# Kernel tuning notes

Hardware: AMD Instinct MI355X
Metric: run time of the kernel (lower is better)

Reference implementation:

```python
import jax, jax.numpy as jnp
import numpy as np

LN2 = 0.693147
TARGET_MEAN = 200.0
TARGET_STD = 40.0
BUFFER_SIZE = 1000
TARGET_LOG_MEAN = float(np.log2(TARGET_MEAN))
TARGET_LOG_STD = TARGET_STD / (TARGET_MEAN * LN2)
BLOCK = 33_554_432  # 2**25 pitch frames


def setup_inputs() -> dict:
    key = jax.random.key(0)
    k1, k2 = jax.random.split(key)
    u = jax.random.uniform(k1, (BLOCK,), dtype=jnp.float32)
    unvoiced = jax.random.uniform(k2, (BLOCK,), dtype=jnp.float32) < 0.2
    # realistic F0 range 80-480 Hz, zeros for unvoiced frames
    pitch = jnp.where(unvoiced, 0.0, 80.0 + 400.0 * u)
    return {"pitch_values": pitch}


def reference(pitch_values):
    # State is the freshly-initialized tracker: empty buffer, buffer_idx = 0.
    N = pitch_values.shape[0]
    B = BUFFER_SIZE
    valid = pitch_values > 0
    # log2 of valid pitches (safe for invalid lanes)
    log_p = jnp.log2(jnp.where(valid, pitch_values, 1.0))

    # rank of each valid element among valid elements (scatter order)
    rank = jnp.cumsum(valid.astype(jnp.int32)) - 1          # [N]
    n_valid = jnp.maximum(rank[-1] + 1, 0)
    # dense array of valid log-pitches ordered by rank (unique indices)
    dense_idx = jnp.where(valid, rank, N)                    # N is OOB -> dropped
    dense = jnp.zeros((N,), pitch_values.dtype).at[dense_idx].set(log_p, mode='drop')

    # circular buffer: slot j holds the LAST (max-rank) value written there
    slot = jnp.where(valid, rank % B, B)                     # B is OOB -> dropped
    winner = jnp.full((B,), -1, jnp.int32).at[slot].max(rank, mode='drop')
    filled = winner >= 0
    buf = jnp.where(filled, dense[jnp.clip(winner, 0, N - 1)], 0.0)

    count = jnp.minimum(n_valid, B)
    cnt_f = jnp.maximum(count, 1).astype(pitch_values.dtype)
    mean = jnp.sum(buf) / cnt_f
    mean = jnp.where(count > 0, mean, 0.0)                   # init mean = 0.0
    var = jnp.sum(jnp.where(filled, (buf - mean) ** 2, 0.0)) / jnp.maximum(count - 1, 1).astype(pitch_values.dtype)
    std = jnp.where(count > 1, jnp.sqrt(var), 1.0)           # unbiased std (torch default)
    std = jnp.maximum(std, 1e-7)

    normalized = (log_p - mean) / std
    scaled = normalized * TARGET_LOG_STD + TARGET_LOG_MEAN
    return jnp.where(valid, jnp.exp2(scaled), 0.0)
```

## Files before the change

### kernel.cpp

```cpp
#include <hip/hip_runtime.h>
#include <math.h>

#define BUF_SIZE 1000
#define TARGET_LOG_MEAN 7.6438561897747395f
#define TARGET_LOG_STD  (40.0f / (200.0f * 0.693147f))

__global__ void stats_kernel(const float* __restrict__ pitch, long long n,
                             float* __restrict__ stats) {
    const int tid = threadIdx.x;
    __shared__ int s_cnt[256];
    __shared__ double s_red[256];

    double sum = 0.0, sumsq = 0.0;
    long long count_so_far = 0;

    const long long nchunks = (n + 1023) >> 10;
    for (long long c = nchunks - 1; c >= 0; --c) {
        const long long base = (c << 10) + (long long)tid * 4;
        float v[4];
        int valid[4];
        int cnt = 0;
#pragma unroll
        for (int j = 0; j < 4; ++j) {
            const long long idx = base + j;
            const float p = (idx < n) ? pitch[idx] : 0.0f;
            v[j] = p;
            valid[j] = (p > 0.0f) ? 1 : 0;
            cnt += valid[j];
        }

        s_cnt[tid] = cnt;
        __syncthreads();
        for (int off = 1; off < 256; off <<= 1) {
            const int mine = s_cnt[tid];
            const int add = (tid >= off) ? s_cnt[tid - off] : 0;
            __syncthreads();
            s_cnt[tid] = mine + add;
            __syncthreads();
        }
        const int incl = s_cnt[tid];
        const int total = s_cnt[255];
        const int suff_after = total - incl;

        int r = 0;
#pragma unroll
        for (int j = 3; j >= 0; --j) {
            if (valid[j]) {
                const long long rev = count_so_far + suff_after + r;
                if (rev < BUF_SIZE) {
                    const double lp = (double)__log2f(v[j]);
                    sum += lp;
                    sumsq += lp * lp;
                }
                r++;
            }
        }

        count_so_far += total;
        __syncthreads();
        if (count_so_far >= BUF_SIZE) break;
    }

    s_red[tid] = sum;
    __syncthreads();
    for (int off = 128; off > 0; off >>= 1) {
        if (tid < off) s_red[tid] += s_red[tid + off];
        __syncthreads();
    }
    const double tsum = s_red[0];
    __syncthreads();
    s_red[tid] = sumsq;
    __syncthreads();
    for (int off = 128; off > 0; off >>= 1) {
        if (tid < off) s_red[tid] += s_red[tid + off];
        __syncthreads();
    }
    const double tsumsq = s_red[0];

    if (tid == 0) {
        const long long count = (count_so_far < BUF_SIZE) ? count_so_far : BUF_SIZE;
        float mean, stdv;
        if (count == 0) {
            mean = 0.0f;
            stdv = 1.0f;
        } else {
            mean = (float)(tsum / (double)count);
            if (count > 1) {
                double var = (tsumsq - tsum * tsum / (double)count) /
                             (double)(count - 1);
                if (var < 0.0) var = 0.0;
                stdv = (float)sqrt(var);
            } else {
                stdv = 1.0f;
            }
        }
        if (stdv < 1e-7f) stdv = 1e-7f;
        const float scale = TARGET_LOG_STD / stdv;
        const float bias = TARGET_LOG_MEAN - mean * scale;
        stats[0] = scale;
        stats[1] = bias;
    }
}

__global__ void apply_kernel(const float4* __restrict__ in4,
                             float4* __restrict__ out4, long long n4,
                             const float* __restrict__ pitch,
                             float* __restrict__ out, long long n,
                             const float* __restrict__ stats) {
    const float scale = stats[0];
    const float bias = stats[1];
    const long long gid = (long long)blockIdx.x * blockDim.x + threadIdx.x;
    const long long stride = (long long)gridDim.x * blockDim.x;

    for (long long k = gid; k < n4; k += stride) {
        const float4 p = in4[k];
        float4 o;
        o.x = (p.x > 0.0f) ? exp2f(fmaf(__log2f(p.x), scale, bias)) : 0.0f;
        o.y = (p.y > 0.0f) ? exp2f(fmaf(__log2f(p.y), scale, bias)) : 0.0f;
        o.z = (p.z > 0.0f) ? exp2f(fmaf(__log2f(p.z), scale, bias)) : 0.0f;
        o.w = (p.w > 0.0f) ? exp2f(fmaf(__log2f(p.w), scale, bias)) : 0.0f;
        out4[k] = o;
    }

    const long long tail_start = n4 * 4;
    for (long long k = tail_start + gid; k < n; k += stride) {
        const float p = pitch[k];
        out[k] = (p > 0.0f) ? exp2f(fmaf(__log2f(p), scale, bias)) : 0.0f;
    }
}

extern "C" void kernel_launch(void* const* d_in, const int* in_sizes, int n_in,
                              void* d_out, int out_size, void* d_ws, size_t ws_size,
                              hipStream_t stream) {
    const float* pitch = (const float*)d_in[0];
    float* out = (float*)d_out;
    const long long n = (long long)in_sizes[0];
    float* stats = (float*)d_ws;

    stats_kernel<<<1, 256, 0, stream>>>(pitch, n, stats);

    const long long n4 = n / 4;
    int blocks = (int)((n4 + 255) / 256);
    if (blocks > 32768) blocks = 32768;
    if (blocks < 1) blocks = 1;
    apply_kernel<<<blocks, 256, 0, stream>>>((const float4*)pitch, (float4*)out,
                                             n4, pitch, out, n, stats);
}
```

Before: 224.8 us.

## Fuse stats and apply kernels with redundant per-block stats and wave ballot scans

Merges the single-block statistics kernel and the elementwise apply kernel into one launch. Each block recomputes the last-1000-valid-element statistics itself, using wave ballots and popcounts in place of the shared-memory Hillis-Steele scan and shuffle reductions in place of the shared tree reductions. The grid is capped at 2048 blocks. This removes a kernel launch and the serialized single-block stats pass, at the cost of every block redundantly reading the tail of the input.

```diff
diff --git a/kernel.cpp b/kernel.cpp
--- a/kernel.cpp
+++ b/kernel.cpp
@@ -5,42 +5,53 @@
 #define TARGET_LOG_MEAN 7.6438561897747395f
 #define TARGET_LOG_STD  (40.0f / (200.0f * 0.693147f))
 
-__global__ void stats_kernel(const float* __restrict__ pitch, long long n,
-                             float* __restrict__ stats) {
-    const int tid = threadIdx.x;
-    __shared__ int s_cnt[256];
-    __shared__ double s_red[256];
+__global__ __launch_bounds__(256) void fused_kernel(
+    const float* __restrict__ pitch, float* __restrict__ out, long long n) {
+    const int tid  = threadIdx.x;
+    const int lane = tid & 63;
+    const int wid  = tid >> 6;
+
+    __shared__ int    s_wtot[4];
+    __shared__ double s_red[8];
+    __shared__ float  s_sb[2];
 
     double sum = 0.0, sumsq = 0.0;
     long long count_so_far = 0;
+
+    const unsigned long long above =
+        (lane == 63) ? 0ULL : (~0ULL << (lane + 1));
 
     const long long nchunks = (n + 1023) >> 10;
     for (long long c = nchunks - 1; c >= 0; --c) {
         const long long base = (c << 10) + (long long)tid * 4;
         float v[4];
         int valid[4];
-        int cnt = 0;
 #pragma unroll
         for (int j = 0; j < 4; ++j) {
             const long long idx = base + j;
             const float p = (idx < n) ? pitch[idx] : 0.0f;
             v[j] = p;
             valid[j] = (p > 0.0f) ? 1 : 0;
-            cnt += valid[j];
         }
 
-        s_cnt[tid] = cnt;
+        int suff_wave = 0;
+        int wtot = 0;
+#pragma unroll
+        for (int j = 0; j < 4; ++j) {
+            const unsigned long long m = __ballot(valid[j]);
+            suff_wave += __popcll(m & above);
+            wtot      += __popcll(m);
+        }
+        if (lane == 0) s_wtot[wid] = wtot;
         __syncthreads();
-        for (int off = 1; off < 256; off <<= 1) {
-            const int mine = s_cnt[tid];
-            const int add = (tid >= off) ? s_cnt[tid - off] : 0;
-            __syncthreads();
-            s_cnt[tid] = mine + add;
-            __syncthreads();
+        int suff_after = suff_wave;
+        int total = 0;
+#pragma unroll
+        for (int w = 0; w < 4; ++w) {
+            const int t = s_wtot[w];
+            total += t;
+            if (w > wid) suff_after += t;
         }
-        const int incl = s_cnt[tid];
-        const int total = s_cnt[255];
-        const int suff_after = total - incl;
 
         int r = 0;
 #pragma unroll
@@ -49,36 +60,29 @@
                 const long long rev = count_so_far + suff_after + r;
                 if (rev < BUF_SIZE) {
                     const double lp = (double)__log2f(v[j]);
-                    sum += lp;
+                    sum   += lp;
                     sumsq += lp * lp;
                 }
                 r++;
             }
         }
-
         count_so_far += total;
         __syncthreads();
         if (count_so_far >= BUF_SIZE) break;
     }
 
-    s_red[tid] = sum;
+#pragma unroll
+    for (int off = 32; off > 0; off >>= 1) {
+        sum   += __shfl_down(sum,   off, 64);
+        sumsq += __shfl_down(sumsq, off, 64);
+    }
+    if (lane == 0) { s_red[wid] = sum; s_red[4 + wid] = sumsq; }
     __syncthreads();
-    for (int off = 128; off > 0; off >>= 1) {
-        if (tid < off) s_red[tid] += s_red[tid + off];
-        __syncthreads();
-    }
-    const double tsum = s_red[0];
-    __syncthreads();
-    s_red[tid] = sumsq;
-    __syncthreads();
-    for (int off = 128; off > 0; off >>= 1) {
-        if (tid < off) s_red[tid] += s_red[tid + off];
-        __syncthreads();
-    }
-    const double tsumsq = s_red[0];
-
     if (tid == 0) {
-        const long long count = (count_so_far < BUF_SIZE) ? count_so_far : BUF_SIZE;
+        const double tsum   = s_red[0] + s_red[1] + s_red[2] + s_red[3];
+        const double tsumsq = s_red[4] + s_red[5] + s_red[6] + s_red[7];
+        const long long count =
+            (count_so_far < BUF_SIZE) ? count_so_far : BUF_SIZE;
         float mean, stdv;
         if (count == 0) {
             mean = 0.0f;
@@ -96,20 +100,17 @@
         }
         if (stdv < 1e-7f) stdv = 1e-7f;
         const float scale = TARGET_LOG_STD / stdv;
-        const float bias = TARGET_LOG_MEAN - mean * scale;
-        stats[0] = scale;
-        stats[1] = bias;
+        s_sb[0] = scale;
+        s_sb[1] = TARGET_LOG_MEAN - mean * scale;
     }
-}
+    __syncthreads();
+    const float scale = s_sb[0];
+    const float bias  = s_sb[1];
 
-__global__ void apply_kernel(const float4* __restrict__ in4,
-                             float4* __restrict__ out4, long long n4,
-                             const float* __restrict__ pitch,
-                             float* __restrict__ out, long long n,
-                             const float* __restrict__ stats) {
-    const float scale = stats[0];
-    const float bias = stats[1];
-    const long long gid = (long long)blockIdx.x * blockDim.x + threadIdx.x;
+    const float4* __restrict__ in4  = (const float4*)pitch;
+    float4* __restrict__       out4 = (float4*)out;
+    const long long n4     = n >> 2;
+    const long long gid    = (long long)blockIdx.x * blockDim.x + tid;
     const long long stride = (long long)gridDim.x * blockDim.x;
 
     for (long long k = gid; k < n4; k += stride) {
@@ -122,7 +123,7 @@
         out4[k] = o;
     }
 
-    const long long tail_start = n4 * 4;
+    const long long tail_start = n4 << 2;
     for (long long k = tail_start + gid; k < n; k += stride) {
         const float p = pitch[k];
         out[k] = (p > 0.0f) ? exp2f(fmaf(__log2f(p), scale, bias)) : 0.0f;
@@ -135,14 +136,12 @@
     const float* pitch = (const float*)d_in[0];
     float* out = (float*)d_out;
     const long long n = (long long)in_sizes[0];
-    float* stats = (float*)d_ws;
 
-    stats_kernel<<<1, 256, 0, stream>>>(pitch, n, stats);
-
+    int blocks = 2048;
     const long long n4 = n / 4;
-    int blocks = (int)((n4 + 255) / 256);
-    if (blocks > 32768) blocks = 32768;
-    if (blocks < 1) blocks = 1;
-    apply_kernel<<<blocks, 256, 0, stream>>>((const float4*)pitch, (float4*)out,
-                                             n4, pitch, out, n, stats);
+    if ((long long)blocks * 256 > n4 + 255) {
+        blocks = (int)((n4 + 255) / 256);
+        if (blocks < 1) blocks = 1;
+    }
+    fused_kernel<<<blocks, 256, 0, stream>>>(pitch, out, n);
 }
```

Result: slower. 233.8 us (+4.0%).
